# Kernel optimization log

Hardware: AMD Instinct MI355X
Metric: run time of the kernel (lower is better)

Reference implementation:

```python
import jax, jax.numpy as jnp
import numpy as np

B, N, D, K, H = 64, 4096, 256, 11, 512
ITERS = 5
EPS = 1e-8
LN_EPS = 1e-5  # torch LayerNorm default
SCALE = D ** -0.5


def _ln(x, w, b):
    m = jnp.mean(x, axis=-1, keepdims=True)
    v = jnp.mean(jnp.square(x - m), axis=-1, keepdims=True)
    return (x - m) * jax.lax.rsqrt(v + LN_EPS) * w + b


def setup_inputs() -> dict:
    key = jax.random.key(0)
    ks = jax.random.split(key, 16)
    s = lambda k, shp, fan: jax.random.normal(k, shp, jnp.float32) * (1.0 / np.sqrt(fan))
    return {
        "inputs": jax.random.normal(ks[0], (B, N, D), jnp.float32),
        "slots_init": jax.random.normal(ks[1], (B, K, D), jnp.float32),
        "ln_f_w": jnp.ones((D,), jnp.float32), "ln_f_b": jnp.zeros((D,), jnp.float32),
        "ln_s_w": jnp.ones((D,), jnp.float32), "ln_s_b": jnp.zeros((D,), jnp.float32),
        "ln_p_w": jnp.ones((D,), jnp.float32), "ln_p_b": jnp.zeros((D,), jnp.float32),
        "Wq": s(ks[2], (D, D), D),
        "Wk": s(ks[3], (D, D), D),
        "Wv": s(ks[4], (D, D), D),
        "W_ih": s(ks[5], (3 * D, D), D), "b_ih": jnp.zeros((3 * D,), jnp.float32),
        "W_hh": s(ks[6], (3 * D, D), D), "b_hh": jnp.zeros((3 * D,), jnp.float32),
        "W1": s(ks[7], (H, D), D), "b1": jnp.zeros((H,), jnp.float32),
        "W2": s(ks[8], (D, H), H), "b2": jnp.zeros((D,), jnp.float32),
    }


def reference(inputs, slots_init, ln_f_w, ln_f_b, ln_s_w, ln_s_b, ln_p_w, ln_p_b,
              Wq, Wk, Wv, W_ih, b_ih, W_hh, b_hh, W1, b1, W2, b2):
    x = _ln(inputs, ln_f_w, ln_f_b)              # (B, N, D)
    k = x @ Wk.T                                  # (B, N, D)
    v = x @ Wv.T                                  # (B, N, D)
    slots = slots_init                            # (B, K, D)
    for _ in range(ITERS):
        slots_prev = slots
        q = _ln(slots, ln_s_w, ln_s_b) @ Wq.T     # (B, K, D)
        dots = jnp.einsum('bid,bjd->bij', q, k) * SCALE  # (B, K, N)
        attn = jax.nn.softmax(dots, axis=1) + EPS        # softmax over slots
        attn = attn / jnp.sum(attn, axis=-1, keepdims=True)
        updates = jnp.einsum('bjd,bij->bid', v, attn)    # (B, K, D)
        # GRUCell (torch semantics)
        gi = updates @ W_ih.T + b_ih              # (B, K, 3D)
        gh = slots_prev @ W_hh.T + b_hh
        i_r, i_z, i_n = jnp.split(gi, 3, axis=-1)
        h_r, h_z, h_n = jnp.split(gh, 3, axis=-1)
        r = jax.nn.sigmoid(i_r + h_r)
        z = jax.nn.sigmoid(i_z + h_z)
        n_ = jnp.tanh(i_n + r * h_n)
        slots = (1.0 - z) * n_ + z * slots_prev
        # residual MLP
        p = _ln(slots, ln_p_w, ln_p_b)
        slots = slots + jnp.maximum(p @ W1.T + b1, 0.0) @ W2.T + b2
    return slots
```

## Files before the change

kernel.cpp:

```cpp
#include <hip/hip_runtime.h>

typedef __bf16 bf16_t;
typedef bf16_t bf16x8 __attribute__((ext_vector_type(8)));
typedef bf16_t bf16x4 __attribute__((ext_vector_type(4)));
typedef float f32x4 __attribute__((ext_vector_type(4)));

#define DEVI static __device__ __forceinline__
#define MFMA16(a, b, c) __builtin_amdgcn_mfma_f32_16x16x32_bf16((a), (b), (c), 0, 0, 0)

constexpr int BB = 64;
constexpr int NN = 4096;
constexpr int DD = 256;
constexpr int KS = 11;
constexpr int KP = 16;
constexpr float EPS_A = 1e-8f;
constexpr float LNEPS = 1e-5f;
constexpr float SCALE = 0.0625f;
constexpr int MR = BB * KP;
constexpr int NSPLIT = 8;
constexpr int ASTR = 40;

DEVI float wredf(float v) {
#pragma unroll
  for (int o = 32; o > 0; o >>= 1) v += __shfl_xor(v, o, 64);
  return v;
}

DEVI float sigm(float x) { return 1.f / (1.f + __expf(-x)); }

__global__ void prep_weights_k(
    const float* __restrict__ s0, const float* __restrict__ s1, const float* __restrict__ s2,
    const float* __restrict__ s3, const float* __restrict__ s4, const float* __restrict__ s5,
    const float* __restrict__ s6,
    bf16_t* d0, bf16_t* d1, bf16_t* d2, bf16_t* d3, bf16_t* d4, bf16_t* d5, bf16_t* d6) {
  int i = blockIdx.x * 256 + threadIdx.x;
  const float* s; bf16_t* d; int o;
  if      (i < 65536)  { s = s0; d = d0; o = i; }
  else if (i < 131072) { s = s1; d = d1; o = i - 65536; }
  else if (i < 196608) { s = s2; d = d2; o = i - 131072; }
  else if (i < 393216) { s = s3; d = d3; o = i - 196608; }
  else if (i < 589824) { s = s4; d = d4; o = i - 393216; }
  else if (i < 720896) { s = s5; d = d5; o = i - 589824; }
  else                 { s = s6; d = d6; o = i - 720896; }
  d[o] = (bf16_t)s[o];
}

__global__ void ln_inputs_k(const float* __restrict__ x, const float* __restrict__ w,
                            const float* __restrict__ bsk, bf16_t* __restrict__ o) {
  const int wvi = threadIdx.x >> 6, lane = threadIdx.x & 63;
  const long row = (long)blockIdx.x * 4 + wvi;
  const float4 v = ((const float4*)(x + row * DD))[lane];
  float s = v.x + v.y + v.z + v.w;
  float s2 = v.x * v.x + v.y * v.y + v.z * v.z + v.w * v.w;
  s = wredf(s); s2 = wredf(s2);
  const float mean = s * (1.f / DD);
  const float var = s2 * (1.f / DD) - mean * mean;
  const float rstd = rsqrtf(var + LNEPS);
  const float4 w4 = ((const float4*)w)[lane];
  const float4 b4 = ((const float4*)bsk)[lane];
  bf16x4 ov;
  ov[0] = (bf16_t)((v.x - mean) * rstd * w4.x + b4.x);
  ov[1] = (bf16_t)((v.y - mean) * rstd * w4.y + b4.y);
  ov[2] = (bf16_t)((v.z - mean) * rstd * w4.z + b4.z);
  ov[3] = (bf16_t)((v.w - mean) * rstd * w4.w + b4.w);
  ((bf16x4*)(o + row * DD))[lane] = ov;
}

__global__ __launch_bounds__(256) void gemm_kv_k(const bf16_t* __restrict__ X,
                                                 const bf16_t* __restrict__ Wk,
                                                 const bf16_t* __restrict__ Wv,
                                                 bf16_t* __restrict__ kout,
                                                 bf16_t* __restrict__ vout) {
  __shared__ bf16_t As[128 * 72];
  __shared__ bf16_t Bs[256 * 72];
  const int bid = blockIdx.x;
  int mode, bx, by;
  if (bid < 2048) { mode = 0; bx = bid & 1023; by = bid >> 10; }
  else            { mode = 1; bx = bid - 2048; by = 0; }
  const bf16_t* Ap; const bf16_t* Bp;
  if (mode == 0) { Ap = Wk + (long)by * 128 * DD; Bp = X + (long)bx * 256 * DD; }
  else           { Ap = X + (long)bx * 128 * DD; Bp = Wv; }
  const int tid = threadIdx.x;
  const int wvi = tid >> 6, lane = tid & 63;
  const int c = lane & 15, q = lane >> 4;
  const int mh = wvi >> 1, nh = wvi & 1;
  f32x4 acc[4][8];
#pragma unroll
  for (int a = 0; a < 4; a++)
#pragma unroll
    for (int b = 0; b < 8; b++) acc[a][b] = (f32x4){0.f, 0.f, 0.f, 0.f};
  for (int kb = 0; kb < DD; kb += 64) {
#pragma unroll
    for (int it = 0; it < 4; ++it) {
      int id = it * 256 + tid, r = id >> 3, ch = id & 7;
      *(bf16x8*)(As + r * 72 + ch * 8) = *(const bf16x8*)(Ap + (long)r * DD + kb + ch * 8);
    }
#pragma unroll
    for (int it = 0; it < 8; ++it) {
      int id = it * 256 + tid, r = id >> 3, ch = id & 7;
      *(bf16x8*)(Bs + r * 72 + ch * 8) = *(const bf16x8*)(Bp + (long)r * DD + kb + ch * 8);
    }
    __syncthreads();
#pragma unroll
    for (int ks = 0; ks < 2; ++ks) {
      bf16x8 af[4], bfr[8];
#pragma unroll
      for (int mt = 0; mt < 4; mt++)
        af[mt] = *(const bf16x8*)(As + (mh * 64 + mt * 16 + c) * 72 + ks * 32 + q * 8);
#pragma unroll
      for (int nt = 0; nt < 8; nt++)
        bfr[nt] = *(const bf16x8*)(Bs + (nh * 128 + nt * 16 + c) * 72 + ks * 32 + q * 8);
#pragma unroll
      for (int mt = 0; mt < 4; mt++)
#pragma unroll
        for (int nt = 0; nt < 8; nt++)
          acc[mt][nt] = MFMA16(af[mt], bfr[nt], acc[mt][nt]);
    }
    __syncthreads();
  }
#pragma unroll
  for (int mt = 0; mt < 4; mt++) {
#pragma unroll
    for (int nt = 0; nt < 8; nt++) {
      bf16x4 o;
#pragma unroll
      for (int r = 0; r < 4; r++) o[r] = (bf16_t)acc[mt][nt][r];
      if (mode == 0) {
        int dg = by * 128 + mh * 64 + mt * 16 + q * 4;
        long ng = (long)bx * 256 + nh * 128 + nt * 16 + c;
        *(bf16x4*)(kout + ng * DD + dg) = o;
      } else {
        long ng = (long)bx * 128 + mh * 64 + mt * 16 + q * 4;
        int d = nh * 128 + nt * 16 + c;
        long b = ng >> 12; int nin = (int)(ng & 4095);
        *(bf16x4*)(vout + (b * DD + d) * NN + nin) = o;
      }
    }
  }
}

__global__ __launch_bounds__(256) void fused_attn_k(const bf16_t* __restrict__ q_bf,
                                                    const bf16_t* __restrict__ k_bf,
                                                    const bf16_t* __restrict__ vT_bf,
                                                    float* __restrict__ upd_part,
                                                    float* __restrict__ rowsum) {
  const int b = blockIdx.x >> 3, sp = blockIdx.x & 7;
  const int wvi = threadIdx.x >> 6, lane = threadIdx.x & 63;
  const int c = lane & 15, q = lane >> 4;

  __shared__ bf16_t att_s[4][16 * ASTR];
  __shared__ float sP[4][KP * DD];
  bf16_t* as = att_s[wvi];

  const bf16_t* qp = q_bf + (long)b * KP * DD;
  bf16x8 af[8];
#pragma unroll
  for (int kc = 0; kc < 8; kc++) af[kc] = *(const bf16x8*)(qp + c * DD + kc * 32 + q * 8);

  f32x4 pacc[16];
#pragma unroll
  for (int dt = 0; dt < 16; dt++) pacc[dt] = (f32x4){0.f, 0.f, 0.f, 0.f};
  float rs[4] = {0.f, 0.f, 0.f, 0.f};

  const int n_base = sp * (NN / NSPLIT) + wvi * 128;
  const bf16_t* kp = k_bf + (long)b * NN * DD;
  const bf16_t* vp = vT_bf + (long)b * DD * NN;

  for (int ch = 0; ch < 4; ++ch) {
    const int n0 = n_base + ch * 32;
    float v[2][4];
#pragma unroll
    for (int t = 0; t < 2; t++) {
      f32x4 dacc = (f32x4){0.f, 0.f, 0.f, 0.f};
      const bf16_t* bp = kp + (long)(n0 + t * 16 + c) * DD + q * 8;
#pragma unroll
      for (int kc = 0; kc < 8; kc++)
        dacc = MFMA16(af[kc], *(const bf16x8*)(bp + kc * 32), dacc);
#pragma unroll
      for (int r = 0; r < 4; r++) {
        float dv = dacc[r] * SCALE;
        if (q * 4 + r >= KS) dv = -1e30f;
        v[t][r] = dv;
      }
      float m4 = fmaxf(fmaxf(v[t][0], v[t][1]), fmaxf(v[t][2], v[t][3]));
      m4 = fmaxf(m4, __shfl_xor(m4, 16, 64));
      m4 = fmaxf(m4, __shfl_xor(m4, 32, 64));
      float s4 = 0.f;
#pragma unroll
      for (int r = 0; r < 4; r++) { v[t][r] = __expf(v[t][r] - m4); s4 += v[t][r]; }
      s4 += __shfl_xor(s4, 16, 64);
      s4 += __shfl_xor(s4, 32, 64);
      const float inv = 1.f / s4;
#pragma unroll
      for (int r = 0; r < 4; r++) {
        float a = v[t][r] * inv + EPS_A;
        rs[r] += a;
        as[(q * 4 + r) * ASTR + t * 16 + c] = (bf16_t)a;
      }
    }
    bf16x8 pa = *(const bf16x8*)(as + c * ASTR + q * 8);
#pragma unroll
    for (int dt = 0; dt < 16; dt++) {
      const bf16_t* bp2 = vp + (long)(dt * 16 + c) * NN + n0 + q * 8;
      pacc[dt] = MFMA16(pa, *(const bf16x8*)(bp2), pacc[dt]);
    }
  }

#pragma unroll
  for (int off = 1; off < 16; off <<= 1)
#pragma unroll
    for (int r = 0; r < 4; r++) rs[r] += __shfl_xor(rs[r], off, 64);
  if (c == 0) {
#pragma unroll
    for (int r = 0; r < 4; r++) atomicAdd(&rowsum[b * KP + q * 4 + r], rs[r]);
  }

#pragma unroll
  for (int dt = 0; dt < 16; dt++)
#pragma unroll
    for (int r = 0; r < 4; r++) sP[wvi][(q * 4 + r) * DD + dt * 16 + c] = pacc[dt][r];
  __syncthreads();
  float* up = upd_part + (long)blockIdx.x * (KP * DD);
  for (int idx = threadIdx.x; idx < KP * DD; idx += 256)
    up[idx] = sP[0][idx] + sP[1][idx] + sP[2][idx] + sP[3][idx];
}

template <int MODE>
__global__ __launch_bounds__(256, 1) void slot_update_k(
    const float* __restrict__ slots_init, float* __restrict__ slots_g,
    const float* __restrict__ upd_part, float* __restrict__ rowsum,
    bf16_t* __restrict__ q_bf, float* __restrict__ d_out,
    const bf16_t* __restrict__ Wq, const bf16_t* __restrict__ Wih,
    const bf16_t* __restrict__ Whh, const bf16_t* __restrict__ W1,
    const bf16_t* __restrict__ W2,
    const float* __restrict__ b_ih, const float* __restrict__ b_hh,
    const float* __restrict__ b1, const float* __restrict__ b2,
    const float* __restrict__ ln_s_w, const float* __restrict__ ln_s_b,
    const float* __restrict__ ln_p_w, const float* __restrict__ ln_p_b) {
  const int b = blockIdx.x;
  const int tid = threadIdx.x, w = tid >> 6, lane = tid & 63;
  const int c = lane & 15, q = lane >> 4;

  __shared__ float sS[16][264];
  __shared__ bf16_t sA1[16 * 272];
  __shared__ bf16_t sA2[16 * 528];
  __shared__ float sMu[16], sRs[16];

  float* slots_b = slots_g + (long)b * KP * DD;

  auto rowstats = [&]() {
    __syncthreads();
    int row = w * 4 + q;
    float sm = 0.f, sq2 = 0.f;
#pragma unroll
    for (int i = 0; i < 16; i++) { float v = sS[row][i * 16 + c]; sm += v; sq2 += v * v; }
#pragma unroll
    for (int o = 1; o < 16; o <<= 1) { sm += __shfl_xor(sm, o, 64); sq2 += __shfl_xor(sq2, o, 64); }
    if (c == 0) {
      float mu = sm * (1.f / 256.f);
      float var = sq2 * (1.f / 256.f) - mu * mu;
      sMu[row] = mu; sRs[row] = rsqrtf(var + LNEPS);
    }
    __syncthreads();
  };

  if constexpr (MODE == 0) {
    for (int idx = tid; idx < KP * DD; idx += 256) {
      int row = idx >> 8, d = idx & 255;
      float v = (row < KS) ? slots_init[((long)b * KS + row) * DD + d] : 0.f;
      sS[row][d] = v;
      slots_b[idx] = v;
    }
  } else {
    for (int idx = tid; idx < KP * DD; idx += 256) {
      int row = idx >> 8, d = idx & 255;
      float sv = slots_b[idx];
      sS[row][d] = sv;
      sA2[row * 272 + d] = (bf16_t)sv;
      float s = 0.f;
      const float* up = upd_part + ((long)b * 8) * (KP * DD) + idx;
#pragma unroll
      for (int p = 0; p < 8; p++) s += up[(long)p * (KP * DD)];
      sA1[row * 272 + d] = (bf16_t)(s / rowsum[b * KP + row]);
    }
    __syncthreads();

    f32x4 air[4], aiz[4], ain[4], ahr[4], ahz[4], ahn[4];
#pragma unroll
    for (int j = 0; j < 4; j++) {
      air[j] = (f32x4){0.f, 0.f, 0.f, 0.f}; aiz[j] = air[j]; ain[j] = air[j];
      ahr[j] = air[j]; ahz[j] = air[j]; ahn[j] = air[j];
    }
    for (int k0 = 0; k0 < 256; k0 += 32) {
      bf16x8 aU = *(const bf16x8*)(sA1 + c * 272 + k0 + q * 8);
      bf16x8 aS = *(const bf16x8*)(sA2 + c * 272 + k0 + q * 8);
#pragma unroll
      for (int j = 0; j < 4; j++) {
        const long colr = (w * 4 + j) * 16 + c;
        air[j] = MFMA16(aU, *(const bf16x8*)(Wih + colr * 256 + k0 + q * 8), air[j]);
        aiz[j] = MFMA16(aU, *(const bf16x8*)(Wih + (colr + 256) * 256 + k0 + q * 8), aiz[j]);
        ain[j] = MFMA16(aU, *(const bf16x8*)(Wih + (colr + 512) * 256 + k0 + q * 8), ain[j]);
        ahr[j] = MFMA16(aS, *(const bf16x8*)(Whh + colr * 256 + k0 + q * 8), ahr[j]);
        ahz[j] = MFMA16(aS, *(const bf16x8*)(Whh + (colr + 256) * 256 + k0 + q * 8), ahz[j]);
        ahn[j] = MFMA16(aS, *(const bf16x8*)(Whh + (colr + 512) * 256 + k0 + q * 8), ahn[j]);
      }
    }
#pragma unroll
    for (int j = 0; j < 4; j++) {
      const int colr = (w * 4 + j) * 16 + c;
      const float bir = b_ih[colr], biz = b_ih[colr + 256], bin = b_ih[colr + 512];
      const float bhr = b_hh[colr], bhz = b_hh[colr + 256], bhn = b_hh[colr + 512];
#pragma unroll
      for (int r = 0; r < 4; r++) {
        const int row = q * 4 + r;
        float rg = sigm(air[j][r] + bir + ahr[j][r] + bhr);
        float zg = sigm(aiz[j][r] + biz + ahz[j][r] + bhz);
        float ng = tanhf(ain[j][r] + bin + rg * (ahn[j][r] + bhn));
        float sp = sS[row][colr];
        sS[row][colr] = (1.f - zg) * ng + zg * sp;
      }
    }

    rowstats();
    for (int idx = tid; idx < KP * DD; idx += 256) {
      int row = idx >> 8, d = idx & 255;
      sA1[row * 272 + d] = (bf16_t)((sS[row][d] - sMu[row]) * sRs[row] * ln_p_w[d] + ln_p_b[d]);
    }
    __syncthreads();

    f32x4 h[8];
#pragma unroll
    for (int j = 0; j < 8; j++) h[j] = (f32x4){0.f, 0.f, 0.f, 0.f};
    for (int k0 = 0; k0 < 256; k0 += 32) {
      bf16x8 aP = *(const bf16x8*)(sA1 + c * 272 + k0 + q * 8);
#pragma unroll
      for (int j = 0; j < 8; j++) {
        const long col = (w * 8 + j) * 16 + c;
        h[j] = MFMA16(aP, *(const bf16x8*)(W1 + col * 256 + k0 + q * 8), h[j]);
      }
    }
#pragma unroll
    for (int j = 0; j < 8; j++) {
      const int col = (w * 8 + j) * 16 + c;
      const float bb = b1[col];
#pragma unroll
      for (int r = 0; r < 4; r++)
        sA2[(q * 4 + r) * 528 + col] = (bf16_t)fmaxf(h[j][r] + bb, 0.f);
    }
    __syncthreads();

    f32x4 m4[4];
#pragma unroll
    for (int j = 0; j < 4; j++) m4[j] = (f32x4){0.f, 0.f, 0.f, 0.f};
    for (int k0 = 0; k0 < 512; k0 += 32) {
      bf16x8 aH = *(const bf16x8*)(sA2 + c * 528 + k0 + q * 8);
#pragma unroll
      for (int j = 0; j < 4; j++) {
        const long col = (w * 4 + j) * 16 + c;
        m4[j] = MFMA16(aH, *(const bf16x8*)(W2 + col * 512 + k0 + q * 8), m4[j]);
      }
    }
#pragma unroll
    for (int j = 0; j < 4; j++) {
      const int col = (w * 4 + j) * 16 + c;
      const float bb = b2[col];
#pragma unroll
      for (int r = 0; r < 4; r++) {
        const int row = q * 4 + r;
        float sfin = m4[j][r] + bb + sS[row][col];
        if constexpr (MODE == 2) {
          if (row < KS) d_out[((long)b * KS + row) * DD + col] = sfin;
        } else {
          sS[row][col] = sfin;
          slots_b[row * DD + col] = sfin;
        }
      }
    }
    if constexpr (MODE == 2) return;
  }

  rowstats();
  for (int idx = tid; idx < KP * DD; idx += 256) {
    int row = idx >> 8, d = idx & 255;
    sA1[row * 272 + d] = (bf16_t)((sS[row][d] - sMu[row]) * sRs[row] * ln_s_w[d] + ln_s_b[d]);
  }
  __syncthreads();

  f32x4 qa[4];
#pragma unroll
  for (int j = 0; j < 4; j++) qa[j] = (f32x4){0.f, 0.f, 0.f, 0.f};
  for (int k0 = 0; k0 < 256; k0 += 32) {
    bf16x8 aL = *(const bf16x8*)(sA1 + c * 272 + k0 + q * 8);
#pragma unroll
    for (int j = 0; j < 4; j++) {
      const long col = (w * 4 + j) * 16 + c;
      qa[j] = MFMA16(aL, *(const bf16x8*)(Wq + col * 256 + k0 + q * 8), qa[j]);
    }
  }
  bf16_t* qb = q_bf + (long)b * KP * DD;
#pragma unroll
  for (int j = 0; j < 4; j++) {
    const int col = (w * 4 + j) * 16 + c;
#pragma unroll
    for (int r = 0; r < 4; r++) qb[(q * 4 + r) * DD + col] = (bf16_t)qa[j][r];
  }
  if (tid < KP) rowsum[b * KP + tid] = 0.f;
}

extern "C" void kernel_launch(void* const* d_in, const int* in_sizes, int n_in, void* d_out,
                              int out_size, void* d_ws, size_t ws_size, hipStream_t stream) {
  (void)in_sizes; (void)n_in; (void)out_size; (void)ws_size;
  const float* inputs = (const float*)d_in[0];
  const float* slots_in = (const float*)d_in[1];
  const float* ln_f_w = (const float*)d_in[2];
  const float* ln_f_b = (const float*)d_in[3];
  const float* ln_s_w = (const float*)d_in[4];
  const float* ln_s_b = (const float*)d_in[5];
  const float* ln_p_w = (const float*)d_in[6];
  const float* ln_p_b = (const float*)d_in[7];
  const float* Wq = (const float*)d_in[8];
  const float* Wk = (const float*)d_in[9];
  const float* Wv = (const float*)d_in[10];
  const float* W_ih = (const float*)d_in[11];
  const float* b_ih = (const float*)d_in[12];
  const float* W_hh = (const float*)d_in[13];
  const float* b_hh = (const float*)d_in[14];
  const float* W1 = (const float*)d_in[15];
  const float* b1 = (const float*)d_in[16];
  const float* W2 = (const float*)d_in[17];
  const float* b2 = (const float*)d_in[18];

  char* p = (char*)d_ws;
  auto alloc = [&](size_t bytes) { char* r = p; p += (bytes + 255) & ~(size_t)255; return r; };
  bf16_t* x_bf  = (bf16_t*)alloc((size_t)BB * NN * DD * 2);
  bf16_t* k_bf  = (bf16_t*)alloc((size_t)BB * NN * DD * 2);
  bf16_t* vT_bf = (bf16_t*)alloc((size_t)BB * NN * DD * 2);
  bf16_t* Wq_bf = (bf16_t*)alloc(65536 * 2);
  bf16_t* Wk_bf = (bf16_t*)alloc(65536 * 2);
  bf16_t* Wv_bf = (bf16_t*)alloc(65536 * 2);
  bf16_t* Wih_bf = (bf16_t*)alloc(196608 * 2);
  bf16_t* Whh_bf = (bf16_t*)alloc(196608 * 2);
  bf16_t* W1_bf = (bf16_t*)alloc(131072 * 2);
  bf16_t* W2_bf = (bf16_t*)alloc(131072 * 2);
  float* slots = (float*)alloc((size_t)MR * DD * 4);
  bf16_t* q_bf = (bf16_t*)alloc((size_t)MR * DD * 2);
  float* upd_part = (float*)alloc((size_t)BB * NSPLIT * KP * DD * 4);
  float* rowsum = (float*)alloc((size_t)MR * 4);

  prep_weights_k<<<3328, 256, 0, stream>>>(Wq, Wk, Wv, W_ih, W_hh, W1, W2, Wq_bf, Wk_bf, Wv_bf,
                                           Wih_bf, Whh_bf, W1_bf, W2_bf);
  slot_update_k<0><<<BB, 256, 0, stream>>>(slots_in, slots, upd_part, rowsum, q_bf, nullptr,
                                           Wq_bf, Wih_bf, Whh_bf, W1_bf, W2_bf,
                                           b_ih, b_hh, b1, b2, ln_s_w, ln_s_b, ln_p_w, ln_p_b);
  ln_inputs_k<<<65536, 256, 0, stream>>>(inputs, ln_f_w, ln_f_b, x_bf);
  gemm_kv_k<<<4096, 256, 0, stream>>>(x_bf, Wk_bf, Wv_bf, k_bf, vT_bf);

  for (int t = 0; t < 5; t++) {
    fused_attn_k<<<BB * NSPLIT, 256, 0, stream>>>(q_bf, k_bf, vT_bf, upd_part, rowsum);
    if (t < 4)
      slot_update_k<1><<<BB, 256, 0, stream>>>(slots_in, slots, upd_part, rowsum, q_bf, nullptr,
                                               Wq_bf, Wih_bf, Whh_bf, W1_bf, W2_bf,
                                               b_ih, b_hh, b1, b2, ln_s_w, ln_s_b, ln_p_w, ln_p_b);
    else
      slot_update_k<2><<<BB, 256, 0, stream>>>(slots_in, slots, upd_part, rowsum, q_bf,
                                               (float*)d_out,
                                               Wq_bf, Wih_bf, Whh_bf, W1_bf, W2_bf,
                                               b_ih, b_hh, b1, b2, ln_s_w, ln_s_b, ln_p_w, ln_p_b);
  }
}
```

Before: 1.346 ms.

## Fuse input LayerNorm into K/V GEMM and restructure attention split across waves

Replaces the separate input LayerNorm kernel and K/V GEMM with one kernel. Each block normalizes 64 rows into shared memory, then computes both K and V^T from that tile, reading weights directly from global memory. This removes the bf16 round trip of the normalized inputs through HBM. The attention kernel doubles the N split to 16 blocks per batch and has waves share a 128-column attention tile through LDS, with each wave owning 64 output dims instead of all 256. That removes the cross-wave shared-memory reduction and cuts accumulator registers, at the cost of an extra barrier per chunk and twice as many partial sums for the slot update to reduce.

Result: faster. 1.244 ms (-7.6%).

```diff
diff --git a/kernel.cpp b/kernel.cpp
--- a/kernel.cpp
+++ b/kernel.cpp
@@ -17,8 +17,8 @@
 constexpr float LNEPS = 1e-5f;
 constexpr float SCALE = 0.0625f;
 constexpr int MR = BB * KP;
-constexpr int NSPLIT = 8;
-constexpr int ASTR = 40;
+constexpr int NSPLIT = 16;
+constexpr int ASTR = 136;
 
 DEVI float wredf(float v) {
 #pragma unroll
@@ -45,97 +45,98 @@
   d[o] = (bf16_t)s[o];
 }
 
-__global__ void ln_inputs_k(const float* __restrict__ x, const float* __restrict__ w,
-                            const float* __restrict__ bsk, bf16_t* __restrict__ o) {
-  const int wvi = threadIdx.x >> 6, lane = threadIdx.x & 63;
-  const long row = (long)blockIdx.x * 4 + wvi;
-  const float4 v = ((const float4*)(x + row * DD))[lane];
-  float s = v.x + v.y + v.z + v.w;
-  float s2 = v.x * v.x + v.y * v.y + v.z * v.z + v.w * v.w;
-  s = wredf(s); s2 = wredf(s2);
-  const float mean = s * (1.f / DD);
-  const float var = s2 * (1.f / DD) - mean * mean;
-  const float rstd = rsqrtf(var + LNEPS);
-  const float4 w4 = ((const float4*)w)[lane];
-  const float4 b4 = ((const float4*)bsk)[lane];
-  bf16x4 ov;
-  ov[0] = (bf16_t)((v.x - mean) * rstd * w4.x + b4.x);
-  ov[1] = (bf16_t)((v.y - mean) * rstd * w4.y + b4.y);
-  ov[2] = (bf16_t)((v.z - mean) * rstd * w4.z + b4.z);
-  ov[3] = (bf16_t)((v.w - mean) * rstd * w4.w + b4.w);
-  ((bf16x4*)(o + row * DD))[lane] = ov;
-}
-
-__global__ __launch_bounds__(256) void gemm_kv_k(const bf16_t* __restrict__ X,
-                                                 const bf16_t* __restrict__ Wk,
-                                                 const bf16_t* __restrict__ Wv,
-                                                 bf16_t* __restrict__ kout,
-                                                 bf16_t* __restrict__ vout) {
-  __shared__ bf16_t As[128 * 72];
-  __shared__ bf16_t Bs[256 * 72];
-  const int bid = blockIdx.x;
-  int mode, bx, by;
-  if (bid < 2048) { mode = 0; bx = bid & 1023; by = bid >> 10; }
-  else            { mode = 1; bx = bid - 2048; by = 0; }
-  const bf16_t* Ap; const bf16_t* Bp;
-  if (mode == 0) { Ap = Wk + (long)by * 128 * DD; Bp = X + (long)bx * 256 * DD; }
-  else           { Ap = X + (long)bx * 128 * DD; Bp = Wv; }
-  const int tid = threadIdx.x;
-  const int wvi = tid >> 6, lane = tid & 63;
+__global__ __launch_bounds__(256) void ln_gemm_kv_k(const float* __restrict__ x,
+                                                    const float* __restrict__ lnw,
+                                                    const float* __restrict__ lnb,
+                                                    const bf16_t* __restrict__ Wk,
+                                                    const bf16_t* __restrict__ Wv,
+                                                    bf16_t* __restrict__ kout,
+                                                    bf16_t* __restrict__ vout) {
+  __shared__ bf16_t xs[64 * 264];
+  const long row0 = (long)blockIdx.x * 64;
+  const int b = (int)(row0 >> 12);
+  const int n0 = (int)(row0 & 4095);
+  const int tid = threadIdx.x, w = tid >> 6, lane = tid & 63;
   const int c = lane & 15, q = lane >> 4;
-  const int mh = wvi >> 1, nh = wvi & 1;
-  f32x4 acc[4][8];
-#pragma unroll
-  for (int a = 0; a < 4; a++)
-#pragma unroll
-    for (int b = 0; b < 8; b++) acc[a][b] = (f32x4){0.f, 0.f, 0.f, 0.f};
-  for (int kb = 0; kb < DD; kb += 64) {
-#pragma unroll
-    for (int it = 0; it < 4; ++it) {
-      int id = it * 256 + tid, r = id >> 3, ch = id & 7;
-      *(bf16x8*)(As + r * 72 + ch * 8) = *(const bf16x8*)(Ap + (long)r * DD + kb + ch * 8);
-    }
-#pragma unroll
-    for (int it = 0; it < 8; ++it) {
-      int id = it * 256 + tid, r = id >> 3, ch = id & 7;
-      *(bf16x8*)(Bs + r * 72 + ch * 8) = *(const bf16x8*)(Bp + (long)r * DD + kb + ch * 8);
-    }
-    __syncthreads();
-#pragma unroll
-    for (int ks = 0; ks < 2; ++ks) {
-      bf16x8 af[4], bfr[8];
+
+#pragma unroll 4
+  for (int pass = 0; pass < 16; ++pass) {
+    const int r = pass * 4 + w;
+    const float4 v = ((const float4*)(x + (row0 + r) * DD))[lane];
+    float s = v.x + v.y + v.z + v.w;
+    float s2 = v.x * v.x + v.y * v.y + v.z * v.z + v.w * v.w;
+    s = wredf(s); s2 = wredf(s2);
+    const float mean = s * (1.f / DD);
+    const float var = s2 * (1.f / DD) - mean * mean;
+    const float rstd = rsqrtf(var + LNEPS);
+    const float4 w4 = ((const float4*)lnw)[lane];
+    const float4 b4 = ((const float4*)lnb)[lane];
+    bf16x4 ov;
+    ov[0] = (bf16_t)((v.x - mean) * rstd * w4.x + b4.x);
+    ov[1] = (bf16_t)((v.y - mean) * rstd * w4.y + b4.y);
+    ov[2] = (bf16_t)((v.z - mean) * rstd * w4.z + b4.z);
+    ov[3] = (bf16_t)((v.w - mean) * rstd * w4.w + b4.w);
+    *(bf16x4*)(xs + r * 264 + lane * 4) = ov;
+  }
+  __syncthreads();
+
+  {
+    f32x4 acc[4][4];
+#pragma unroll
+    for (int mt = 0; mt < 4; mt++)
+#pragma unroll
+      for (int j = 0; j < 4; j++) acc[mt][j] = (f32x4){0.f, 0.f, 0.f, 0.f};
+    for (int k0 = 0; k0 < 256; k0 += 32) {
+      bf16x8 bfr[4];
+#pragma unroll
+      for (int j = 0; j < 4; j++)
+        bfr[j] = *(const bf16x8*)(xs + (j * 16 + c) * 264 + k0 + q * 8);
+#pragma unroll
+      for (int mt = 0; mt < 4; mt++) {
+        bf16x8 af = *(const bf16x8*)(Wk + (long)(w * 64 + mt * 16 + c) * 256 + k0 + q * 8);
+#pragma unroll
+        for (int j = 0; j < 4; j++) acc[mt][j] = MFMA16(af, bfr[j], acc[mt][j]);
+      }
+    }
+#pragma unroll
+    for (int mt = 0; mt < 4; mt++)
+#pragma unroll
+      for (int j = 0; j < 4; j++) {
+        bf16x4 o;
+#pragma unroll
+        for (int r = 0; r < 4; r++) o[r] = (bf16_t)acc[mt][j][r];
+        *(bf16x4*)(kout + (row0 + j * 16 + c) * DD + w * 64 + mt * 16 + q * 4) = o;
+      }
+  }
+
+  {
+    f32x4 acc[4][4];
+#pragma unroll
+    for (int mt = 0; mt < 4; mt++)
+#pragma unroll
+      for (int j = 0; j < 4; j++) acc[mt][j] = (f32x4){0.f, 0.f, 0.f, 0.f};
+    for (int k0 = 0; k0 < 256; k0 += 32) {
+      bf16x8 af[4];
 #pragma unroll
       for (int mt = 0; mt < 4; mt++)
-        af[mt] = *(const bf16x8*)(As + (mh * 64 + mt * 16 + c) * 72 + ks * 32 + q * 8);
-#pragma unroll
-      for (int nt = 0; nt < 8; nt++)
-        bfr[nt] = *(const bf16x8*)(Bs + (nh * 128 + nt * 16 + c) * 72 + ks * 32 + q * 8);
-#pragma unroll
-      for (int mt = 0; mt < 4; mt++)
-#pragma unroll
-        for (int nt = 0; nt < 8; nt++)
-          acc[mt][nt] = MFMA16(af[mt], bfr[nt], acc[mt][nt]);
-    }
-    __syncthreads();
-  }
-#pragma unroll
-  for (int mt = 0; mt < 4; mt++) {
-#pragma unroll
-    for (int nt = 0; nt < 8; nt++) {
-      bf16x4 o;
-#pragma unroll
-      for (int r = 0; r < 4; r++) o[r] = (bf16_t)acc[mt][nt][r];
-      if (mode == 0) {
-        int dg = by * 128 + mh * 64 + mt * 16 + q * 4;
-        long ng = (long)bx * 256 + nh * 128 + nt * 16 + c;
-        *(bf16x4*)(kout + ng * DD + dg) = o;
-      } else {
-        long ng = (long)bx * 128 + mh * 64 + mt * 16 + q * 4;
-        int d = nh * 128 + nt * 16 + c;
-        long b = ng >> 12; int nin = (int)(ng & 4095);
-        *(bf16x4*)(vout + (b * DD + d) * NN + nin) = o;
-      }
-    }
+        af[mt] = *(const bf16x8*)(xs + (mt * 16 + c) * 264 + k0 + q * 8);
+#pragma unroll
+      for (int j = 0; j < 4; j++) {
+        bf16x8 bfr = *(const bf16x8*)(Wv + (long)(w * 64 + j * 16 + c) * 256 + k0 + q * 8);
+#pragma unroll
+        for (int mt = 0; mt < 4; mt++) acc[mt][j] = MFMA16(af[mt], bfr, acc[mt][j]);
+      }
+    }
+#pragma unroll
+    for (int mt = 0; mt < 4; mt++)
+#pragma unroll
+      for (int j = 0; j < 4; j++) {
+        bf16x4 o;
+#pragma unroll
+        for (int r = 0; r < 4; r++) o[r] = (bf16_t)acc[mt][j][r];
+        const int d = w * 64 + j * 16 + c;
+        *(bf16x4*)(vout + ((long)b * DD + d) * NN + n0 + mt * 16 + q * 4) = o;
+      }
   }
 }
 
@@ -144,65 +145,71 @@
                                                     const bf16_t* __restrict__ vT_bf,
                                                     float* __restrict__ upd_part,
                                                     float* __restrict__ rowsum) {
-  const int b = blockIdx.x >> 3, sp = blockIdx.x & 7;
-  const int wvi = threadIdx.x >> 6, lane = threadIdx.x & 63;
+  const int b = blockIdx.x / NSPLIT, sp = blockIdx.x % NSPLIT;
+  const int w = threadIdx.x >> 6, lane = threadIdx.x & 63;
   const int c = lane & 15, q = lane >> 4;
 
-  __shared__ bf16_t att_s[4][16 * ASTR];
-  __shared__ float sP[4][KP * DD];
-  bf16_t* as = att_s[wvi];
+  __shared__ bf16_t att_s[2][16 * ASTR];
 
   const bf16_t* qp = q_bf + (long)b * KP * DD;
   bf16x8 af[8];
 #pragma unroll
   for (int kc = 0; kc < 8; kc++) af[kc] = *(const bf16x8*)(qp + c * DD + kc * 32 + q * 8);
 
-  f32x4 pacc[16];
-#pragma unroll
-  for (int dt = 0; dt < 16; dt++) pacc[dt] = (f32x4){0.f, 0.f, 0.f, 0.f};
+  f32x4 pacc[4];
+#pragma unroll
+  for (int j = 0; j < 4; j++) pacc[j] = (f32x4){0.f, 0.f, 0.f, 0.f};
   float rs[4] = {0.f, 0.f, 0.f, 0.f};
 
-  const int n_base = sp * (NN / NSPLIT) + wvi * 128;
+  const int nb0 = sp * (NN / NSPLIT);
   const bf16_t* kp = k_bf + (long)b * NN * DD;
   const bf16_t* vp = vT_bf + (long)b * DD * NN;
 
-  for (int ch = 0; ch < 4; ++ch) {
-    const int n0 = n_base + ch * 32;
-    float v[2][4];
+  for (int chunk = 0; chunk < 2; ++chunk) {
+    const int n0 = nb0 + chunk * 128;
+    const int nw = n0 + w * 32;
+    bf16_t* as = att_s[chunk & 1];
 #pragma unroll
     for (int t = 0; t < 2; t++) {
-      f32x4 dacc = (f32x4){0.f, 0.f, 0.f, 0.f};
-      const bf16_t* bp = kp + (long)(n0 + t * 16 + c) * DD + q * 8;
-#pragma unroll
-      for (int kc = 0; kc < 8; kc++)
-        dacc = MFMA16(af[kc], *(const bf16x8*)(bp + kc * 32), dacc);
+      const bf16_t* bp = kp + (long)(nw + t * 16 + c) * DD + q * 8;
+      f32x4 d0 = (f32x4){0.f, 0.f, 0.f, 0.f}, d1 = (f32x4){0.f, 0.f, 0.f, 0.f};
+#pragma unroll
+      for (int kc = 0; kc < 4; kc++) {
+        d0 = MFMA16(af[2 * kc],     *(const bf16x8*)(bp + kc * 64),      d0);
+        d1 = MFMA16(af[2 * kc + 1], *(const bf16x8*)(bp + kc * 64 + 32), d1);
+      }
+      float v[4];
 #pragma unroll
       for (int r = 0; r < 4; r++) {
-        float dv = dacc[r] * SCALE;
+        float dv = (d0[r] + d1[r]) * SCALE;
         if (q * 4 + r >= KS) dv = -1e30f;
-        v[t][r] = dv;
-      }
-      float m4 = fmaxf(fmaxf(v[t][0], v[t][1]), fmaxf(v[t][2], v[t][3]));
+        v[r] = dv;
+      }
+      float m4 = fmaxf(fmaxf(v[0], v[1]), fmaxf(v[2], v[3]));
       m4 = fmaxf(m4, __shfl_xor(m4, 16, 64));
       m4 = fmaxf(m4, __shfl_xor(m4, 32, 64));
       float s4 = 0.f;
 #pragma unroll
-      for (int r = 0; r < 4; r++) { v[t][r] = __expf(v[t][r] - m4); s4 += v[t][r]; }
+      for (int r = 0; r < 4; r++) { v[r] = __expf(v[r] - m4); s4 += v[r]; }
       s4 += __shfl_xor(s4, 16, 64);
       s4 += __shfl_xor(s4, 32, 64);
       const float inv = 1.f / s4;
 #pragma unroll
       for (int r = 0; r < 4; r++) {
-        float a = v[t][r] * inv + EPS_A;
+        float a = v[r] * inv + EPS_A;
         rs[r] += a;
-        as[(q * 4 + r) * ASTR + t * 16 + c] = (bf16_t)a;
-      }
-    }
-    bf16x8 pa = *(const bf16x8*)(as + c * ASTR + q * 8);
-#pragma unroll
-    for (int dt = 0; dt < 16; dt++) {
-      const bf16_t* bp2 = vp + (long)(dt * 16 + c) * NN + n0 + q * 8;
-      pacc[dt] = MFMA16(pa, *(const bf16x8*)(bp2), pacc[dt]);
+        as[(q * 4 + r) * ASTR + (w * 32 + t * 16 + c)] = (bf16_t)a;
+      }
+    }
+    __syncthreads();
+#pragma unroll
+    for (int ns = 0; ns < 4; ns++) {
+      bf16x8 pa = *(const bf16x8*)(as + c * ASTR + ns * 32 + q * 8);
+#pragma unroll
+      for (int j = 0; j < 4; j++) {
+        const bf16_t* bp2 = vp + (long)(w * 64 + j * 16 + c) * NN + n0 + ns * 32 + q * 8;
+        pacc[j] = MFMA16(pa, *(const bf16x8*)bp2, pacc[j]);
+      }
     }
   }
 
@@ -215,18 +222,15 @@
     for (int r = 0; r < 4; r++) atomicAdd(&rowsum[b * KP + q * 4 + r], rs[r]);
   }
 
-#pragma unroll
-  for (int dt = 0; dt < 16; dt++)
-#pragma unroll
-    for (int r = 0; r < 4; r++) sP[wvi][(q * 4 + r) * DD + dt * 16 + c] = pacc[dt][r];
-  __syncthreads();
   float* up = upd_part + (long)blockIdx.x * (KP * DD);
-  for (int idx = threadIdx.x; idx < KP * DD; idx += 256)
-    up[idx] = sP[0][idx] + sP[1][idx] + sP[2][idx] + sP[3][idx];
+#pragma unroll
+  for (int j = 0; j < 4; j++)
+#pragma unroll
+    for (int r = 0; r < 4; r++) up[(q * 4 + r) * DD + w * 64 + j * 16 + c] = pacc[j][r];
 }
 
 template <int MODE>
-__global__ __launch_bounds__(256, 1) void slot_update_k(
+__global__ __launch_bounds__(256) void slot_update_k(
     const float* __restrict__ slots_init, float* __restrict__ slots_g,
     const float* __restrict__ upd_part, float* __restrict__ rowsum,
     bf16_t* __restrict__ q_bf, float* __restrict__ d_out,
@@ -278,9 +282,9 @@
       sS[row][d] = sv;
       sA2[row * 272 + d] = (bf16_t)sv;
       float s = 0.f;
-      const float* up = upd_part + ((long)b * 8) * (KP * DD) + idx;
-#pragma unroll
-      for (int p = 0; p < 8; p++) s += up[(long)p * (KP * DD)];
+      const float* up = upd_part + ((long)b * NSPLIT) * (KP * DD) + idx;
+#pragma unroll
+      for (int p = 0; p < NSPLIT; p++) s += up[(long)p * (KP * DD)];
       sA1[row * 272 + d] = (bf16_t)(s / rowsum[b * KP + row]);
     }
     __syncthreads();
@@ -432,7 +436,6 @@
 
   char* p = (char*)d_ws;
   auto alloc = [&](size_t bytes) { char* r = p; p += (bytes + 255) & ~(size_t)255; return r; };
-  bf16_t* x_bf  = (bf16_t*)alloc((size_t)BB * NN * DD * 2);
   bf16_t* k_bf  = (bf16_t*)alloc((size_t)BB * NN * DD * 2);
   bf16_t* vT_bf = (bf16_t*)alloc((size_t)BB * NN * DD * 2);
   bf16_t* Wq_bf = (bf16_t*)alloc(65536 * 2);
@@ -452,8 +455,7 @@
   slot_update_k<0><<<BB, 256, 0, stream>>>(slots_in, slots, upd_part, rowsum, q_bf, nullptr,
                                            Wq_bf, Wih_bf, Whh_bf, W1_bf, W2_bf,
                                            b_ih, b_hh, b1, b2, ln_s_w, ln_s_b, ln_p_w, ln_p_b);
-  ln_inputs_k<<<65536, 256, 0, stream>>>(inputs, ln_f_w, ln_f_b, x_bf);
-  gemm_kv_k<<<4096, 256, 0, stream>>>(x_bf, Wk_bf, Wv_bf, k_bf, vT_bf);
+  ln_gemm_kv_k<<<BB * NN / 64, 256, 0, stream>>>(inputs, ln_f_w, ln_f_b, Wk_bf, Wv_bf, k_bf, vT_bf);
 
   for (int t = 0; t < 5; t++) {
     fused_attn_k<<<BB * NSPLIT, 256, 0, stream>>>(q_bf, k_bf, vT_bf, upd_part, rowsum);
```
